# Kernel optimization log

Hardware: AMD Instinct MI355X
Metric: run time of the kernel (lower is better)

## Reference

```python
import jax, jax.numpy as jnp
import numpy as np
from jax import lax

B, C_IN, C_OUT, K, W_DIM, H, W = 16, 512, 512, 3, 512, 64, 64


def setup_inputs() -> dict:
    key = jax.random.key(0)
    k1, k2, k3, k4, k5 = jax.random.split(key, 5)
    fan_in = C_IN * K * K
    bound = 1.0 / np.sqrt(fan_in)
    imgs = jax.random.normal(k1, (B, C_IN, H, W), dtype=jnp.float32)
    w_embs = jax.random.normal(k2, (B, W_DIM), dtype=jnp.float32)
    conv_weight = jax.random.uniform(k3, (C_OUT, C_IN, K, K), jnp.float32, -bound, bound)
    conv_bias = jax.random.uniform(k4, (C_OUT,), jnp.float32, -bound, bound)
    sb = 1.0 / np.sqrt(W_DIM)
    style_W = jax.random.uniform(k5, (C_IN, W_DIM), jnp.float32, -sb, sb)
    style_b = jnp.zeros((C_IN,), jnp.float32)
    return {"imgs": imgs, "w_embs": w_embs, "conv_weight": conv_weight,
            "conv_bias": conv_bias, "style_W": style_W, "style_b": style_b}


def reference(imgs, w_embs, conv_weight, conv_bias, style_W, style_b):
    b, c, h, w = imgs.shape
    out_dim, in_dim, ky, kx = conv_weight.shape
    # style modulation: (b, in_dim), +1 as in the torch module
    style = w_embs @ style_W.T + style_b + 1.0
    # per-sample weights: (b, out_dim, in_dim, ky, kx)
    weight = conv_weight[None] * style[:, None, :, None, None]
    # demodulation: exact L2 norm over (in_dim, ky, kx) (no eps, matching torch)
    norm = jnp.sqrt(jnp.sum(weight * weight, axis=(2, 3, 4), keepdims=True))
    weight = weight / norm
    # grouped conv with groups = batch
    x = imgs.reshape(1, b * c, h, w)
    k = weight.reshape(b * out_dim, in_dim, ky, kx)
    y = lax.conv_general_dilated(
        x, k, window_strides=(1, 1), padding="SAME",
        feature_group_count=b,
        dimension_numbers=("NCHW", "OIHW", "NCHW"))
    y = y.reshape(b, out_dim, h, w)
    return y + conv_bias[None, :, None, None]
```

## Files before the change

### kernel.cpp

```cpp
#include <hip/hip_runtime.h>


typedef __bf16 bf16x8 __attribute__((ext_vector_type(8)));
typedef float f32x4 __attribute__((ext_vector_type(4)));

__device__ __forceinline__ void async16(const void* g, void* s) {
  __builtin_amdgcn_global_load_lds((const __attribute__((address_space(1))) void*)g,
                                   (__attribute__((address_space(3))) void*)s, 16, 0, 0);
}

__global__ __launch_bounds__(256) void k_style(const float* __restrict__ we,
                                               const float* __restrict__ sW,
                                               const float* __restrict__ sb,
                                               float* __restrict__ style) {
  int lane = threadIdx.x & 63, wid = threadIdx.x >> 6;
  int b = blockIdx.x >> 7;
  int i = ((blockIdx.x & 127) << 2) + wid;
  const float* wer = we + b * 512;
  const float* swr = sW + i * 512;
  float acc = 0.f;
  for (int d = lane; d < 512; d += 64) acc += wer[d] * swr[d];
#pragma unroll
  for (int off = 32; off; off >>= 1) acc += __shfl_xor(acc, off);
  if (lane == 0) style[b * 512 + i] = acc + sb[i] + 1.0f;
}

__global__ __launch_bounds__(256) void k_wsq(const float* __restrict__ cw,
                                             float* __restrict__ wsq) {
  int t = blockIdx.x * 256 + threadIdx.x;
  const float* p = cw + (long)t * 9;
  float s = 0.f;
#pragma unroll
  for (int k = 0; k < 9; ++k) s += p[k] * p[k];
  wsq[t] = s;
}

__global__ __launch_bounds__(256) void k_rnorm(const float* __restrict__ style,
                                               const float* __restrict__ wsq,
                                               float* __restrict__ rnorm) {
  int lane = threadIdx.x & 63, wid = threadIdx.x >> 6;
  int idx = blockIdx.x * 4 + wid;
  int b = idx >> 9, o = idx & 511;
  float acc = 0.f;
  for (int i = lane; i < 512; i += 64) {
    float s = style[(b << 9) + i];
    acc += s * s * wsq[(o << 9) + i];
  }
#pragma unroll
  for (int off = 32; off; off >>= 1) acc += __shfl_xor(acc, off);
  if (lane == 0) rnorm[idx] = rsqrtf(acc);
}

__global__ __launch_bounds__(256) void k_wt(const float* __restrict__ cw,
                                            const float* __restrict__ style,
                                            const float* __restrict__ rnorm,
                                            __bf16* __restrict__ wt) {
  int t = blockIdx.x * 256 + threadIdx.x;
  int b = t >> 18;
  int oi = t & 262143;
  int o = oi >> 9, i = oi & 511;
  float sc = style[(b << 9) + i] * rnorm[(b << 9) + o];
  const float* p = cw + (long)oi * 9;
#pragma unroll
  for (int k = 0; k < 9; ++k) {
    int tp = (k % 3) * 3 + k / 3;
    wt[((long)(b * 9 + tp) << 18) + ((long)o << 9) + i] = (__bf16)(p[k] * sc);
  }
}

__global__ __launch_bounds__(256) void k_xpad(const float* __restrict__ imgs,
                                              __bf16* __restrict__ xpad) {
  int t = blockIdx.x * 256 + threadIdx.x;
  if (t >= 16 * 4356) return;
  int b = t / 4356;
  int rc = t - b * 4356;
  int r = rc / 66, c = rc - (rc / 66) * 66;
  __bf16* dst = xpad + (long)t * 512;
  if (r == 0 || r == 65 || c == 0 || c == 65) {
    const f32x4 z = {0.f, 0.f, 0.f, 0.f};
#pragma unroll 4
    for (int j = 0; j < 64; ++j) *(f32x4*)(dst + j * 8) = z;
  } else {
    const float* src = imgs + ((long)b << 21) + ((r - 1) << 6) + (c - 1);
    for (int j = 0; j < 64; ++j) {
      bf16x8 v;
#pragma unroll
      for (int q = 0; q < 8; ++q) v[q] = (__bf16)src[(long)(j * 8 + q) << 12];
      *(bf16x8*)(dst + j * 8) = v;
    }
  }
}

__global__ __launch_bounds__(256, 2) void k_conv(const __bf16* __restrict__ xpad,
                                                 const __bf16* __restrict__ wt,
                                                 const float* __restrict__ bias,
                                                 float* __restrict__ out) {
  __shared__ __attribute__((aligned(16))) __bf16 sX[2816 * 8];
  __shared__ __attribute__((aligned(16))) __bf16 sA3[3 * 128 * 32];

  const int tid = threadIdx.x;
  const int lane = tid & 63;
  const int wid = tid >> 6;
  const int wr = wid >> 1, wp = wid & 1;
  const int l15 = lane & 15, lq = lane >> 4;

  const int bid0 = blockIdx.x;
  const int bid = ((bid0 & 7) << 7) | (bid0 >> 3);

  const int b = bid >> 6;
  const int r6 = bid & 63;
  const int o0 = (r6 >> 4) << 7;
  const int st = r6 & 15;
  const int h0 = (st >> 1) << 3;
  const int w0 = (st & 1) << 5;
  const int b66 = b * 66;

  const __bf16* xg[11];
#pragma unroll
  for (int it = 0; it < 11; ++it) {
    int s = it * 256 + tid;
    if (s > 2719) s = 2719;
    int p = s >> 3;
    int j = (s & 7) ^ (p & 7);
    int lr = p / 34, lc = p - (p / 34) * 34;
    xg[it] = xpad + ((long)((b66 + h0 + lr) * 66) + (w0 + lc)) * 512 + j * 8;
  }
  const int abase = ((o0 + (tid >> 2)) << 9) + (((tid & 3) ^ ((tid >> 3) & 3)) << 3);
  const __bf16* wtb = wt + (long)b * 2359296;

  f32x4 acc[4][8];
  const f32x4 zero4 = {0.f, 0.f, 0.f, 0.f};
#pragma unroll
  for (int m = 0; m < 4; ++m)
#pragma unroll
    for (int n = 0; n < 8; ++n) acc[m][n] = zero4;

  const int arowbase = (wr << 6) + l15;
  const int csA = (lq ^ ((l15 >> 1) & 3)) << 3;
  const int rbase = wp << 2;

  bool first = true;
  for (int icb = 0; icb < 8; ++icb) {
    const int ic = icb << 6;
#pragma unroll
    for (int hf = 0; hf < 2; ++hf) {
#pragma unroll
      for (int kx = 0; kx < 3; ++kx) {
        if (!first) __syncthreads();
        first = false;
        if (hf == 0 && kx == 0) {
#pragma unroll
          for (int it = 0; it < 11; ++it)
            async16(xg[it] + ic, (char*)sX + it * 4096 + (wid << 10));
        }
        {
          const __bf16* wa = wtb + abase + ic + (hf << 5);
#pragma unroll
          for (int it = 0; it < 6; ++it)
            async16(wa + (kx * 3 + (it >> 1)) * 262144 + (it & 1) * 32768,
                    (char*)sA3 + it * 4096 + (wid << 10));
        }
        __syncthreads();
        const int jb = (hf << 2) | lq;
        bf16x8 bfr[6][2];
#pragma unroll
        for (int r = 0; r < 6; ++r)
#pragma unroll
          for (int c = 0; c < 2; ++c) {
            int p = (rbase + r) * 34 + (c << 4) + l15 + kx;
            bfr[r][c] = *(const bf16x8*)&sX[(p << 6) + ((jb ^ (p & 7)) << 3)];
          }
#pragma unroll
        for (int ky = 0; ky < 3; ++ky) {
          const __bf16* sAb = sA3 + ky * 4096;
          bf16x8 af[4];
#pragma unroll
          for (int m = 0; m < 4; ++m)
            af[m] = *(const bf16x8*)&sAb[((arowbase + (m << 4)) << 5) + csA];
#pragma unroll
          for (int m = 0; m < 4; ++m)
#pragma unroll
            for (int n = 0; n < 8; ++n)
              acc[m][n] = __builtin_amdgcn_mfma_f32_16x16x32_bf16(
                  af[m], bfr[(n >> 1) + ky][n & 1], acc[m][n], 0, 0, 0);
        }
      }
    }
  }

  float* outb = out + ((long)b << 21);
#pragma unroll
  for (int m = 0; m < 4; ++m) {
    int ob = o0 + (wr << 6) + (m << 4) + (lq << 2);
#pragma unroll
    for (int n = 0; n < 8; ++n) {
      int pid = (wp << 7) + (n << 4) + l15;
      int h = h0 + (pid >> 5), w = w0 + (pid & 31);
#pragma unroll
      for (int q = 0; q < 4; ++q) {
        int o = ob + q;
        outb[((long)o << 12) + (h << 6) + w] = acc[m][n][q] + bias[o];
      }
    }
  }
}

extern "C" void kernel_launch(void* const* d_in, const int* in_sizes, int n_in,
                              void* d_out, int out_size, void* d_ws, size_t ws_size,
                              hipStream_t stream) {
  const float* imgs = (const float*)d_in[0];
  const float* w_embs = (const float*)d_in[1];
  const float* cw = (const float*)d_in[2];
  const float* bias = (const float*)d_in[3];
  const float* style_W = (const float*)d_in[4];
  const float* style_b = (const float*)d_in[5];
  float* out = (float*)d_out;

  char* ws = (char*)d_ws;
  float* style = (float*)(ws);
  float* rnorm = (float*)(ws + (32 << 10));
  float* wsq = (float*)(ws + (64 << 10));
  __bf16* wt = (__bf16*)(ws + (64 << 10) + (1 << 20));
  __bf16* xpad = (__bf16*)(ws + (64 << 10) + (1 << 20) + 75497472);
  size_t need = (size_t)(64 << 10) + (1 << 20) + 75497472ull + 71368704ull;
  if (ws_size < need) return;

  k_style<<<2048, 256, 0, stream>>>(w_embs, style_W, style_b, style);
  k_wsq<<<1024, 256, 0, stream>>>(cw, wsq);
  k_rnorm<<<2048, 256, 0, stream>>>(style, wsq, rnorm);
  k_wt<<<16384, 256, 0, stream>>>(cw, style, rnorm, wt);
  k_xpad<<<273, 256, 0, stream>>>(imgs, xpad);
  k_conv<<<1024, 256, 0, stream>>>(xpad, wt, bias, out);
}
```

Before: 372.5 us.

## Double-buffer weight tiles and stream input channels per half-step

The weight tile buffer is split into two ping-pong halves. The next kx or half-channel slice is prefetched asynchronously while MFMAs run on the current one, with explicit vmcnt waits replacing the full load-then-sync pattern. The input tile now holds only 32 channels at a time, with a new swizzle, and is refilled after each kx==2 step. This shrinks the X buffer enough to make room for the second weight buffer. The aim is to hide global-to-LDS latency behind compute, at the cost of tighter hand-managed ordering across barriers and waitcnts.

```diff
diff --git a/kernel.cpp b/kernel.cpp
--- a/kernel.cpp
+++ b/kernel.cpp
@@ -95,8 +95,8 @@
                                                  const __bf16* __restrict__ wt,
                                                  const float* __restrict__ bias,
                                                  float* __restrict__ out) {
-  __shared__ __attribute__((aligned(16))) __bf16 sX[2816 * 8];
-  __shared__ __attribute__((aligned(16))) __bf16 sA3[3 * 128 * 32];
+  __shared__ __attribute__((aligned(16))) __bf16 sX[1536 * 8];
+  __shared__ __attribute__((aligned(16))) __bf16 sA3[2 * 3 * 128 * 32];
 
   const int tid = threadIdx.x;
   const int lane = tid & 63;
@@ -115,13 +115,13 @@
   const int w0 = (st & 1) << 5;
   const int b66 = b * 66;
 
-  const __bf16* xg[11];
-#pragma unroll
-  for (int it = 0; it < 11; ++it) {
+  const __bf16* xg[6];
+#pragma unroll
+  for (int it = 0; it < 6; ++it) {
     int s = it * 256 + tid;
-    if (s > 2719) s = 2719;
-    int p = s >> 3;
-    int j = (s & 7) ^ (p & 7);
+    if (s > 1359) s = 1359;
+    int p = s >> 2;
+    int j = (s & 3) ^ ((p >> 1) & 3);
     int lr = p / 34, lc = p - (p / 34) * 34;
     xg[it] = xpad + ((long)((b66 + h0 + lr) * 66) + (w0 + lc)) * 512 + j * 8;
   }
@@ -139,40 +139,51 @@
   const int csA = (lq ^ ((l15 >> 1) & 3)) << 3;
   const int rbase = wp << 2;
 
-  bool first = true;
+#pragma unroll
+  for (int it = 0; it < 6; ++it)
+    async16(xg[it], (char*)sX + it * 4096 + (wid << 10));
+#pragma unroll
+  for (int it = 0; it < 6; ++it)
+    async16(wtb + abase + (it >> 1) * 262144 + (it & 1) * 32768,
+            (char*)sA3 + it * 4096 + (wid << 10));
+
   for (int icb = 0; icb < 8; ++icb) {
-    const int ic = icb << 6;
 #pragma unroll
     for (int hf = 0; hf < 2; ++hf) {
 #pragma unroll
       for (int kx = 0; kx < 3; ++kx) {
-        if (!first) __syncthreads();
-        first = false;
-        if (hf == 0 && kx == 0) {
-#pragma unroll
-          for (int it = 0; it < 11; ++it)
-            async16(xg[it] + ic, (char*)sX + it * 4096 + (wid << 10));
-        }
-        {
-          const __bf16* wa = wtb + abase + ic + (hf << 5);
+        const int bufc = (3 * hf + kx) & 1;
+        __builtin_amdgcn_sched_barrier(0);
+        __builtin_amdgcn_s_barrier();
+        const bool last = (icb == 7) && (hf == 1) && (kx == 2);
+        if (!last) {
+          const int nkx = (kx == 2) ? 0 : kx + 1;
+          const int nhf = (kx == 2) ? (hf ^ 1) : hf;
+          const int nicb = icb + ((kx == 2 && hf == 1) ? 1 : 0);
+          const __bf16* wa = wtb + abase + (nicb << 6) + (nhf << 5);
+          char* dst = (char*)sA3 + ((bufc ^ 1) * 24576) + (wid << 10);
 #pragma unroll
           for (int it = 0; it < 6; ++it)
-            async16(wa + (kx * 3 + (it >> 1)) * 262144 + (it & 1) * 32768,
-                    (char*)sA3 + it * 4096 + (wid << 10));
-        }
-        __syncthreads();
-        const int jb = (hf << 2) | lq;
+            async16(wa + (nkx * 3 + (it >> 1)) * 262144 + (it & 1) * 32768,
+                    dst + it * 4096);
+        }
+        if (last) {
+          asm volatile("s_waitcnt vmcnt(0)" ::: "memory");
+        } else {
+          asm volatile("s_waitcnt vmcnt(6)" ::: "memory");
+        }
+        __builtin_amdgcn_sched_barrier(0);
         bf16x8 bfr[6][2];
 #pragma unroll
         for (int r = 0; r < 6; ++r)
 #pragma unroll
           for (int c = 0; c < 2; ++c) {
             int p = (rbase + r) * 34 + (c << 4) + l15 + kx;
-            bfr[r][c] = *(const bf16x8*)&sX[(p << 6) + ((jb ^ (p & 7)) << 3)];
+            bfr[r][c] = *(const bf16x8*)&sX[(p << 5) + ((lq ^ ((p >> 1) & 3)) << 3)];
           }
 #pragma unroll
         for (int ky = 0; ky < 3; ++ky) {
-          const __bf16* sAb = sA3 + ky * 4096;
+          const __bf16* sAb = sA3 + bufc * 12288 + ky * 4096;
           bf16x8 af[4];
 #pragma unroll
           for (int m = 0; m < 4; ++m)
@@ -183,6 +194,14 @@
             for (int n = 0; n < 8; ++n)
               acc[m][n] = __builtin_amdgcn_mfma_f32_16x16x32_bf16(
                   af[m], bfr[(n >> 1) + ky][n & 1], acc[m][n], 0, 0, 0);
+        }
+        if (kx == 2 && !last) {
+          __builtin_amdgcn_sched_barrier(0);
+          __builtin_amdgcn_s_barrier();
+          const int chX = ((icb + hf) << 6) + ((hf ^ 1) << 5);
+#pragma unroll
+          for (int it = 0; it < 6; ++it)
+            async16(xg[it] + chX, (char*)sX + it * 4096 + (wid << 10));
         }
       }
     }
```

Result: slower. 434.1 us (+16.5%).
